# Kernel tuning notes

Measured on AMD Instinct MI355X. Metric: run time of the kernel, lower is better.

The kernel has to match this reference:

```python
import jax, jax.numpy as jnp
import numpy as np
from jax import lax

# SLAYER SRMALPHA neuron / simulation constants (from init params)
THETA = 10.0      # spike threshold
TAU_SR = 10.0     # synaptic (PSP) alpha-kernel time constant
TAU_REF = 1.0     # refractory alpha-kernel time constant
SCALE_REF = 2.0   # refractory kernel scale (x theta)
TS = 1.0          # simulation timestep


def _alpha_filter(x, tau):
    """Causal convolution of x[T, ...] with the SLAYER alpha kernel
    k[n] = (n*TS/tau) * exp(1 - n*TS/tau)  (note k[0] = 0),
    implemented as a 2-state linear recurrence (exact, O(T)).
    k[n] = c * n * a**n with a = exp(-TS/tau), c = e*TS/tau.
    """
    a = jnp.asarray(np.exp(-TS / tau), x.dtype)
    c = jnp.asarray(np.e * TS / tau, x.dtype)

    def step(carry, xn):
        p, q = carry              # p[n-1] = sum a^{n-1-m} x[m]; q[n-1] = sum (n-1-m) a^{n-1-m} x[m]
        q = a * q + a * p         # q[n]
        p = a * p + xn            # p[n]
        return (p, q), c * q      # y[n] = c*q[n]  (x[n] has weight k[0]=0)

    z = jnp.zeros_like(x[0])
    _, y = lax.scan(step, (z, z), x)
    return y


def _spike_with_refractory(u):
    """SLAYER spike: threshold membrane potential u[T, B, O]; each emitted
    spike injects the refractory alpha kernel -scaleRef*theta*(t/tauRef)*exp(1-t/tauRef)
    into the future membrane potential. Same 2-state alpha recurrence, but the
    filtered signal is the (data-dependent) spike train -> sequential scan.
    """
    a = jnp.asarray(np.exp(-TS / TAU_REF), u.dtype)
    c = jnp.asarray(-SCALE_REF * THETA * np.e * TS / TAU_REF, u.dtype)

    def step(carry, un):
        p, q = carry
        q = a * q + a * p                       # refractory trace of past spikes
        s = (un + c * q >= THETA).astype(un.dtype)
        p = a * p + s
        return (p, q), s

    z = jnp.zeros_like(u[0])
    _, s = lax.scan(step, (z, z), u)
    return s


def setup_inputs() -> dict:
    key = jax.random.key(0)
    k1, k2 = jax.random.split(key)
    B, CIN, COUT, T = 32, 1024, 1024, 500
    spike_input = (jax.random.uniform(k1, (B, CIN, 1, 1, T)) < 0.05).astype(jnp.float32)
    W = jax.random.normal(k2, (COUT, CIN), dtype=jnp.float32) * (1.0 / np.sqrt(CIN))
    return {"spike_input": spike_input, "W": W}


def reference(spike_input, W):
    B, C, _, _, T = spike_input.shape
    O = W.shape[0]
    x = spike_input.reshape(B, C, T).transpose(2, 0, 1)   # [T, B, C]
    psp = _alpha_filter(x, TAU_SR)                        # temporal PSP filter
    u = jnp.einsum('tbc,oc->tbo', psp, W)                 # slayer.dense = 1x1 conv = GEMM
    s = _spike_with_refractory(u)                         # threshold + refractory
    return s.transpose(1, 2, 0).reshape(B, O, 1, 1, T)
```

## Files before the change

kernel.cpp:

```cpp
#include <hip/hip_runtime.h>
#include <cstddef>
#include <cstdint>

#define T_DIM 500
#define B_DIM 32
#define C_DIM 1024
#define O_DIM 1024
#define M_DIM (T_DIM * B_DIM)
#define MP_DIM 16128
#define BO_DIM (B_DIM * O_DIM)

typedef __attribute__((ext_vector_type(8))) short bf16x8;
typedef __attribute__((ext_vector_type(4))) float f32x4;

static __device__ __forceinline__ ushort f2bf(float x) {
  unsigned u = __float_as_uint(x);
  return (ushort)((u + 0x7FFF + ((u >> 16) & 1)) >> 16);
}
static __device__ __forceinline__ float bf2f(ushort u) {
  return __uint_as_float(((unsigned)u) << 16);
}

static __device__ __forceinline__ bf16x8 ldsr(const ushort* p) {
  bf16x8 d;
  asm volatile("ds_read_b128 %0, %1"
               : "=v"(d)
               : "v"((unsigned)(uintptr_t)(const __attribute__((address_space(3))) ushort*)p));
  return d;
}

__global__ __launch_bounds__(256) void k_transpose(const float* __restrict__ x,
                                                   ushort* __restrict__ xt) {
  __shared__ float tile[32][33];
  const int b  = blockIdx.z;
  const int t0 = blockIdx.x * 32;
  const int c0 = blockIdx.y * 32;
  const int tx = threadIdx.x;
  const int ty = threadIdx.y;

  const int t = t0 + tx;
  if (t < T_DIM) {
#pragma unroll
    for (int r = 0; r < 4; ++r) {
      const int c = c0 + ty + r * 8;
      tile[ty + r * 8][tx] = x[((size_t)b * C_DIM + c) * T_DIM + t];
    }
  }
  __syncthreads();
#pragma unroll
  for (int r = 0; r < 4; ++r) {
    const int tt = t0 + ty + r * 8;
    if (tt < T_DIM) {
      xt[((size_t)tt * B_DIM + b) * C_DIM + c0 + tx] = f2bf(tile[tx][ty + r * 8]);
    }
  }
}

__global__ __launch_bounds__(256) void k_cast_w(const float4* __restrict__ W,
                                                ushort* __restrict__ Wb) {
  const int i = blockIdx.x * 256 + threadIdx.x;
  const float4 w = W[i];
  ushort* o = Wb + (size_t)i * 4;
  o[0] = f2bf(w.x); o[1] = f2bf(w.y); o[2] = f2bf(w.z); o[3] = f2bf(w.w);
}

__global__ __launch_bounds__(512, 2) void k_gemm_bf16(const ushort* __restrict__ A,
                                                      const ushort* __restrict__ Bw,
                                                      ushort* __restrict__ C) {
  __shared__ ushort lds[65536];

  const int tid  = threadIdx.x;
  const int wid  = tid >> 6;
  const int lane = tid & 63;

  const int orig = blockIdx.x;
  const int xcd  = orig & 7;
  const int base = (xcd < 4) ? xcd * 32 : 128 + (xcd - 4) * 31;
  const int wgid = base + (orig >> 3);
  const int row0 = (wgid >> 2) * 256;
  const int col0 = (wgid & 3) * 256;

  const int wm = wid >> 2;
  const int wn = wid & 3;

  f32x4 acc[8][4] = {};

  const int srow = wid * 16 + (lane >> 2);
  const int skof = ((lane & 3) * 8) ^ (((lane >> 5) & 1) << 4);
  const ushort* Abase = A  + (size_t)(row0 + srow) * C_DIM + skof;
  const ushort* Bbase = Bw + (size_t)(col0 + srow) * C_DIM + skof;

  const int fr  = lane & 15;
  const int fko = ((lane >> 4) * 8) ^ (((lane >> 3) & 1) << 4);
  const int aoff = wm * 8192 + fr * 32 + fko;
  const int boff = 16384 + (wn >> 1) * 8192 + (wn & 1) * 2048 + fr * 32 + fko;

#define STAGE_A(K0S, SB)                                                          \
  _Pragma("unroll")                                                               \
  for (int rh = 0; rh < 2; ++rh)                                                  \
    _Pragma("unroll")                                                             \
    for (int kh = 0; kh < 2; ++kh)                                                \
      __builtin_amdgcn_global_load_lds(                                           \
          (const __attribute__((address_space(1))) void*)(Abase + (size_t)rh * 128 * C_DIM + (K0S) + kh * 32), \
          (__attribute__((address_space(3))) void*)&lds[(SB) + rh * 8192 + kh * 4096 + wid * 512], 16, 0, 0)

#define STAGE_B(K0S, SB)                                                          \
  _Pragma("unroll")                                                               \
  for (int rh = 0; rh < 2; ++rh)                                                  \
    _Pragma("unroll")                                                             \
    for (int kh = 0; kh < 2; ++kh)                                                \
      __builtin_amdgcn_global_load_lds(                                           \
          (const __attribute__((address_space(1))) void*)(Bbase + (size_t)rh * 128 * C_DIM + (K0S) + kh * 32), \
          (__attribute__((address_space(3))) void*)&lds[(SB) + 16384 + rh * 8192 + kh * 4096 + wid * 512], 16, 0, 0)

  STAGE_A(0, 0);
  STAGE_B(0, 0);
  STAGE_A(64, 32768);
  STAGE_B(64, 32768);

  for (int t = 0; t < 16; ++t) {
    const int sb = (t & 1) * 32768;
    bf16x8 a0[4][2], a1[4][2], b0[2][2], b1[2][2];

    if (t < 15) { asm volatile("s_waitcnt vmcnt(8)" ::: "memory"); }
    else        { asm volatile("s_waitcnt vmcnt(0)" ::: "memory"); }
    __builtin_amdgcn_s_barrier();
#pragma unroll
    for (int i = 0; i < 4; ++i)
#pragma unroll
      for (int h = 0; h < 2; ++h)
        a0[i][h] = ldsr(&lds[sb + aoff + h * 4096 + i * 512]);
#pragma unroll
    for (int j = 0; j < 2; ++j)
#pragma unroll
      for (int h = 0; h < 2; ++h)
        b0[j][h] = ldsr(&lds[sb + boff + h * 4096 + j * 512]);
    asm volatile("s_waitcnt lgkmcnt(0)" ::: "memory");
    __builtin_amdgcn_sched_barrier(0);
    __builtin_amdgcn_s_setprio(1);
#pragma unroll
    for (int i = 0; i < 4; ++i)
#pragma unroll
      for (int j = 0; j < 2; ++j)
#pragma unroll
        for (int h = 0; h < 2; ++h)
          acc[i][j] = __builtin_amdgcn_mfma_f32_16x16x32_bf16(a0[i][h], b0[j][h], acc[i][j], 0, 0, 0);
    __builtin_amdgcn_s_setprio(0);
    __builtin_amdgcn_s_barrier();

#pragma unroll
    for (int i = 0; i < 4; ++i)
#pragma unroll
      for (int h = 0; h < 2; ++h)
        a1[i][h] = ldsr(&lds[sb + aoff + h * 4096 + (4 + i) * 512]);
#pragma unroll
    for (int j = 0; j < 2; ++j)
#pragma unroll
      for (int h = 0; h < 2; ++h)
        b1[j][h] = ldsr(&lds[sb + boff + h * 4096 + (2 + j) * 512]);
    asm volatile("s_waitcnt lgkmcnt(0)" ::: "memory");
    __builtin_amdgcn_sched_barrier(0);
    __builtin_amdgcn_s_setprio(1);
#pragma unroll
    for (int i = 0; i < 4; ++i)
#pragma unroll
      for (int j = 0; j < 2; ++j)
#pragma unroll
        for (int h = 0; h < 2; ++h)
          acc[4 + i][j] = __builtin_amdgcn_mfma_f32_16x16x32_bf16(a1[i][h], b0[j][h], acc[4 + i][j], 0, 0, 0);
    __builtin_amdgcn_s_setprio(0);
    __builtin_amdgcn_s_barrier();

    if (t < 14) { STAGE_A((t + 2) * 64, sb); }
    __builtin_amdgcn_s_setprio(1);
#pragma unroll
    for (int i = 0; i < 4; ++i)
#pragma unroll
      for (int j = 0; j < 2; ++j)
#pragma unroll
        for (int h = 0; h < 2; ++h)
          acc[i][2 + j] = __builtin_amdgcn_mfma_f32_16x16x32_bf16(a0[i][h], b1[j][h], acc[i][2 + j], 0, 0, 0);
    __builtin_amdgcn_s_setprio(0);
    __builtin_amdgcn_s_barrier();

    if (t < 14) { STAGE_B((t + 2) * 64, sb); }
    __builtin_amdgcn_s_setprio(1);
#pragma unroll
    for (int i = 0; i < 4; ++i)
#pragma unroll
      for (int j = 0; j < 2; ++j)
#pragma unroll
        for (int h = 0; h < 2; ++h)
          acc[4 + i][2 + j] = __builtin_amdgcn_mfma_f32_16x16x32_bf16(a1[i][h], b1[j][h], acc[4 + i][2 + j], 0, 0, 0);
    __builtin_amdgcn_s_setprio(0);
    __builtin_amdgcn_s_barrier();
  }

  const int crow = (lane >> 4) * 4;
  const int ccol = lane & 15;
#pragma unroll
  for (int i = 0; i < 8; ++i)
#pragma unroll
    for (int j = 0; j < 4; ++j) {
      ushort* cp = C + (size_t)(row0 + wm * 128 + i * 16 + crow) * O_DIM
                     + (col0 + wn * 64 + j * 16 + ccol);
#pragma unroll
      for (int r = 0; r < 4; ++r) cp[(size_t)r * O_DIM] = f2bf(acc[i][j][r]);
    }
#undef STAGE_A
#undef STAGE_B
}

__global__ __launch_bounds__(64) void k_scan(const ushort* __restrict__ v,
                                             float* __restrict__ out) {
  const int g = blockIdx.x * 64 + threadIdx.x;

  const float a1 = 0.90483741803595952f;
  const float c1 = 0.27182818284590452f;
  const float a2 = 0.36787944117144233f;
  const float c2 = -54.365636569180905f;

  float p1 = 0.f, q1 = 0.f;
  float p2 = 0.f, q2 = 0.f;

  const ushort* vp = v + g;
  float* op = out + (size_t)g * T_DIM;

  constexpr int D  = 20;
  constexpr int NC = 25;

  ushort b0[D], b1[D], b2[D];
#pragma unroll
  for (int j = 0; j < D; ++j) b0[j] = vp[(size_t)j * BO_DIM];
#pragma unroll
  for (int j = 0; j < D; ++j) b1[j] = vp[(size_t)(D + j) * BO_DIM];
#pragma unroll
  for (int j = 0; j < D; ++j) b2[j] = vp[(size_t)(2 * D + j) * BO_DIM];

#pragma unroll 5
  for (int c = 0; c < NC; ++c) {
    const int cn = (c + 3 < NC) ? (c + 3) : (NC - 1);
    ushort bn[D];
    {
      const size_t base = (size_t)cn * D;
#pragma unroll
      for (int j = 0; j < D; ++j) bn[j] = vp[(base + j) * BO_DIM];
    }

    float rr[D];
#pragma unroll
    for (int j = 0; j < D; ++j) {
      const float vn = bf2f(b0[j]);
      q1 = a1 * q1 + a1 * p1;
      p1 = a1 * p1 + vn;
      const float u = c1 * q1;
      q2 = a2 * q2 + a2 * p2;
      const float s = (u + c2 * q2 >= 10.0f) ? 1.0f : 0.0f;
      p2 = a2 * p2 + s;
      rr[j] = s;
    }

    float* o = op + c * D;
#pragma unroll
    for (int j = 0; j < D; j += 4)
      *(float4*)&o[j] = make_float4(rr[j], rr[j + 1], rr[j + 2], rr[j + 3]);

#pragma unroll
    for (int j = 0; j < D; ++j) { b0[j] = b1[j]; b1[j] = b2[j]; b2[j] = bn[j]; }
  }
}

extern "C" void kernel_launch(void* const* d_in, const int* in_sizes, int n_in,
                              void* d_out, int out_size, void* d_ws, size_t ws_size,
                              hipStream_t stream) {
  const float* x = (const float*)d_in[0];
  const float* W = (const float*)d_in[1];
  float* out = (float*)d_out;

  ushort* v  = (ushort*)d_ws;
  ushort* xt = v + (size_t)MP_DIM * O_DIM;
  ushort* Wb = xt + (size_t)MP_DIM * C_DIM;

  dim3 g0((T_DIM + 31) / 32, C_DIM / 32, B_DIM);
  k_transpose<<<g0, dim3(32, 8), 0, stream>>>(x, xt);

  k_cast_w<<<(O_DIM * C_DIM / 4) / 256, 256, 0, stream>>>((const float4*)W, Wb);

  k_gemm_bf16<<<(MP_DIM / 256) * (O_DIM / 256), 512, 0, stream>>>(xt, Wb, v);

  k_scan<<<BO_DIM / 64, 64, 0, stream>>>(v, out);
}
```

Baseline: 90.05 us.

## Double GEMM workgroup to 1024 threads and coalesce scan output via LDS bitmasks

The GEMM keeps its 256x256 tile but splits it across 16 waves instead of 8. Each wave now owns 64x64 outputs, which halves the accumulator registers and issues one K-half load per thread. The scan packs spike bits into per-thread LDS words and then writes each output row cooperatively, so the scattered per-thread stores of stride-500 rows become coalesced float4 writes. Costs include more barrier participants, the launch-bounds request of 1024 threads with 4 blocks (which LDS size cannot actually satisfy), and a clamped tail read in the scan.

```diff
diff --git a/kernel.cpp b/kernel.cpp
--- a/kernel.cpp
+++ b/kernel.cpp
@@ -64,9 +64,9 @@
   o[0] = f2bf(w.x); o[1] = f2bf(w.y); o[2] = f2bf(w.z); o[3] = f2bf(w.w);
 }
 
-__global__ __launch_bounds__(512, 2) void k_gemm_bf16(const ushort* __restrict__ A,
-                                                      const ushort* __restrict__ Bw,
-                                                      ushort* __restrict__ C) {
+__global__ __launch_bounds__(1024, 4) void k_gemm_bf16(const ushort* __restrict__ A,
+                                                       const ushort* __restrict__ Bw,
+                                                       ushort* __restrict__ C) {
   __shared__ ushort lds[65536];
 
   const int tid  = threadIdx.x;
@@ -83,35 +83,32 @@
   const int wm = wid >> 2;
   const int wn = wid & 3;
 
-  f32x4 acc[8][4] = {};
-
-  const int srow = wid * 16 + (lane >> 2);
-  const int skof = ((lane & 3) * 8) ^ (((lane >> 5) & 1) << 4);
-  const ushort* Abase = A  + (size_t)(row0 + srow) * C_DIM + skof;
-  const ushort* Bbase = Bw + (size_t)(col0 + srow) * C_DIM + skof;
+  f32x4 acc[4][4] = {};
+
+  const int kh  = tid >> 9;
+  const int rin = (tid >> 2) & 127;
+  const int sk  = ((tid & 3) * 8) ^ (((tid >> 5) & 1) << 4);
+  const ushort* Abase = A  + (size_t)(row0 + rin) * C_DIM + kh * 32 + sk;
+  const ushort* Bbase = Bw + (size_t)(col0 + rin) * C_DIM + kh * 32 + sk;
 
   const int fr  = lane & 15;
   const int fko = ((lane >> 4) * 8) ^ (((lane >> 3) & 1) << 4);
-  const int aoff = wm * 8192 + fr * 32 + fko;
-  const int boff = 16384 + (wn >> 1) * 8192 + (wn & 1) * 2048 + fr * 32 + fko;
+  const int aoff = (wm >> 1) * 8192 + ((wm & 1) * 64 + fr) * 32 + fko;
+  const int boff = 16384 + (wn >> 1) * 8192 + ((wn & 1) * 64 + fr) * 32 + fko;
 
 #define STAGE_A(K0S, SB)                                                          \
   _Pragma("unroll")                                                               \
   for (int rh = 0; rh < 2; ++rh)                                                  \
-    _Pragma("unroll")                                                             \
-    for (int kh = 0; kh < 2; ++kh)                                                \
-      __builtin_amdgcn_global_load_lds(                                           \
-          (const __attribute__((address_space(1))) void*)(Abase + (size_t)rh * 128 * C_DIM + (K0S) + kh * 32), \
-          (__attribute__((address_space(3))) void*)&lds[(SB) + rh * 8192 + kh * 4096 + wid * 512], 16, 0, 0)
+    __builtin_amdgcn_global_load_lds(                                             \
+        (const __attribute__((address_space(1))) void*)(Abase + (size_t)rh * 128 * C_DIM + (K0S)), \
+        (__attribute__((address_space(3))) void*)&lds[(SB) + rh * 8192 + wid * 512], 16, 0, 0)
 
 #define STAGE_B(K0S, SB)                                                          \
   _Pragma("unroll")                                                               \
   for (int rh = 0; rh < 2; ++rh)                                                  \
-    _Pragma("unroll")                                                             \
-    for (int kh = 0; kh < 2; ++kh)                                                \
-      __builtin_amdgcn_global_load_lds(                                           \
-          (const __attribute__((address_space(1))) void*)(Bbase + (size_t)rh * 128 * C_DIM + (K0S) + kh * 32), \
-          (__attribute__((address_space(3))) void*)&lds[(SB) + 16384 + rh * 8192 + kh * 4096 + wid * 512], 16, 0, 0)
+    __builtin_amdgcn_global_load_lds(                                             \
+        (const __attribute__((address_space(1))) void*)(Bbase + (size_t)rh * 128 * C_DIM + (K0S)), \
+        (__attribute__((address_space(3))) void*)&lds[(SB) + 16384 + rh * 8192 + wid * 512], 16, 0, 0)
 
   STAGE_A(0, 0);
   STAGE_B(0, 0);
@@ -120,16 +117,16 @@
 
   for (int t = 0; t < 16; ++t) {
     const int sb = (t & 1) * 32768;
-    bf16x8 a0[4][2], a1[4][2], b0[2][2], b1[2][2];
-
-    if (t < 15) { asm volatile("s_waitcnt vmcnt(8)" ::: "memory"); }
+    bf16x8 a[4][2], b0[2][2], b1[2][2];
+
+    if (t < 15) { asm volatile("s_waitcnt vmcnt(4)" ::: "memory"); }
     else        { asm volatile("s_waitcnt vmcnt(0)" ::: "memory"); }
     __builtin_amdgcn_s_barrier();
 #pragma unroll
     for (int i = 0; i < 4; ++i)
 #pragma unroll
       for (int h = 0; h < 2; ++h)
-        a0[i][h] = ldsr(&lds[sb + aoff + h * 4096 + i * 512]);
+        a[i][h] = ldsr(&lds[sb + aoff + h * 4096 + i * 512]);
 #pragma unroll
     for (int j = 0; j < 2; ++j)
 #pragma unroll
@@ -139,20 +136,15 @@
     __builtin_amdgcn_sched_barrier(0);
     __builtin_amdgcn_s_setprio(1);
 #pragma unroll
-    for (int i = 0; i < 4; ++i)
+    for (int i = 0; i < 2; ++i)
 #pragma unroll
       for (int j = 0; j < 2; ++j)
 #pragma unroll
         for (int h = 0; h < 2; ++h)
-          acc[i][j] = __builtin_amdgcn_mfma_f32_16x16x32_bf16(a0[i][h], b0[j][h], acc[i][j], 0, 0, 0);
+          acc[i][j] = __builtin_amdgcn_mfma_f32_16x16x32_bf16(a[i][h], b0[j][h], acc[i][j], 0, 0, 0);
     __builtin_amdgcn_s_setprio(0);
     __builtin_amdgcn_s_barrier();
 
-#pragma unroll
-    for (int i = 0; i < 4; ++i)
-#pragma unroll
-      for (int h = 0; h < 2; ++h)
-        a1[i][h] = ldsr(&lds[sb + aoff + h * 4096 + (4 + i) * 512]);
 #pragma unroll
     for (int j = 0; j < 2; ++j)
 #pragma unroll
@@ -162,36 +154,36 @@
     __builtin_amdgcn_sched_barrier(0);
     __builtin_amdgcn_s_setprio(1);
 #pragma unroll
-    for (int i = 0; i < 4; ++i)
+    for (int i = 2; i < 4; ++i)
 #pragma unroll
       for (int j = 0; j < 2; ++j)
 #pragma unroll
         for (int h = 0; h < 2; ++h)
-          acc[4 + i][j] = __builtin_amdgcn_mfma_f32_16x16x32_bf16(a1[i][h], b0[j][h], acc[4 + i][j], 0, 0, 0);
+          acc[i][j] = __builtin_amdgcn_mfma_f32_16x16x32_bf16(a[i][h], b0[j][h], acc[i][j], 0, 0, 0);
     __builtin_amdgcn_s_setprio(0);
     __builtin_amdgcn_s_barrier();
 
     if (t < 14) { STAGE_A((t + 2) * 64, sb); }
     __builtin_amdgcn_s_setprio(1);
 #pragma unroll
-    for (int i = 0; i < 4; ++i)
+    for (int i = 0; i < 2; ++i)
 #pragma unroll
       for (int j = 0; j < 2; ++j)
 #pragma unroll
         for (int h = 0; h < 2; ++h)
-          acc[i][2 + j] = __builtin_amdgcn_mfma_f32_16x16x32_bf16(a0[i][h], b1[j][h], acc[i][2 + j], 0, 0, 0);
+          acc[i][2 + j] = __builtin_amdgcn_mfma_f32_16x16x32_bf16(a[i][h], b1[j][h], acc[i][2 + j], 0, 0, 0);
     __builtin_amdgcn_s_setprio(0);
     __builtin_amdgcn_s_barrier();
 
     if (t < 14) { STAGE_B((t + 2) * 64, sb); }
     __builtin_amdgcn_s_setprio(1);
 #pragma unroll
-    for (int i = 0; i < 4; ++i)
+    for (int i = 2; i < 4; ++i)
 #pragma unroll
       for (int j = 0; j < 2; ++j)
 #pragma unroll
         for (int h = 0; h < 2; ++h)
-          acc[4 + i][2 + j] = __builtin_amdgcn_mfma_f32_16x16x32_bf16(a1[i][h], b1[j][h], acc[4 + i][2 + j], 0, 0, 0);
+          acc[i][2 + j] = __builtin_amdgcn_mfma_f32_16x16x32_bf16(a[i][h], b1[j][h], acc[i][2 + j], 0, 0, 0);
     __builtin_amdgcn_s_setprio(0);
     __builtin_amdgcn_s_barrier();
   }
@@ -199,10 +191,10 @@
   const int crow = (lane >> 4) * 4;
   const int ccol = lane & 15;
 #pragma unroll
-  for (int i = 0; i < 8; ++i)
+  for (int i = 0; i < 4; ++i)
 #pragma unroll
     for (int j = 0; j < 4; ++j) {
-      ushort* cp = C + (size_t)(row0 + wm * 128 + i * 16 + crow) * O_DIM
+      ushort* cp = C + (size_t)(row0 + wm * 64 + i * 16 + crow) * O_DIM
                      + (col0 + wn * 64 + j * 16 + ccol);
 #pragma unroll
       for (int r = 0; r < 4; ++r) cp[(size_t)r * O_DIM] = f2bf(acc[i][j][r]);
@@ -213,7 +205,9 @@
 
 __global__ __launch_bounds__(64) void k_scan(const ushort* __restrict__ v,
                                              float* __restrict__ out) {
-  const int g = blockIdx.x * 64 + threadIdx.x;
+  __shared__ unsigned wbits[64][16];
+  const int l  = threadIdx.x;
+  const int g0 = blockIdx.x * 64;
 
   const float a1 = 0.90483741803595952f;
   const float c1 = 0.27182818284590452f;
@@ -223,11 +217,10 @@
   float p1 = 0.f, q1 = 0.f;
   float p2 = 0.f, q2 = 0.f;
 
-  const ushort* vp = v + g;
-  float* op = out + (size_t)g * T_DIM;
-
-  constexpr int D  = 20;
-  constexpr int NC = 25;
+  const ushort* vp = v + g0 + l;
+
+  constexpr int D  = 32;
+  constexpr int NC = 16;
 
   ushort b0[D], b1[D], b2[D];
 #pragma unroll
@@ -237,17 +230,18 @@
 #pragma unroll
   for (int j = 0; j < D; ++j) b2[j] = vp[(size_t)(2 * D + j) * BO_DIM];
 
-#pragma unroll 5
+#pragma unroll 4
   for (int c = 0; c < NC; ++c) {
     const int cn = (c + 3 < NC) ? (c + 3) : (NC - 1);
     ushort bn[D];
-    {
-      const size_t base = (size_t)cn * D;
-#pragma unroll
-      for (int j = 0; j < D; ++j) bn[j] = vp[(base + j) * BO_DIM];
-    }
-
-    float rr[D];
+#pragma unroll
+    for (int j = 0; j < D; ++j) {
+      int t = cn * D + j;
+      if (t > 499) t = 499;
+      bn[j] = vp[(size_t)t * BO_DIM];
+    }
+
+    unsigned curw = 0;
 #pragma unroll
     for (int j = 0; j < D; ++j) {
       const float vn = bf2f(b0[j]);
@@ -255,18 +249,34 @@
       p1 = a1 * p1 + vn;
       const float u = c1 * q1;
       q2 = a2 * q2 + a2 * p2;
-      const float s = (u + c2 * q2 >= 10.0f) ? 1.0f : 0.0f;
-      p2 = a2 * p2 + s;
-      rr[j] = s;
-    }
-
-    float* o = op + c * D;
-#pragma unroll
-    for (int j = 0; j < D; j += 4)
-      *(float4*)&o[j] = make_float4(rr[j], rr[j + 1], rr[j + 2], rr[j + 3]);
+      const bool fire = (u + c2 * q2 >= 10.0f);
+      p2 = a2 * p2 + (fire ? 1.0f : 0.0f);
+      curw |= (unsigned)fire << j;
+    }
+    wbits[l][c] = curw;
 
 #pragma unroll
     for (int j = 0; j < D; ++j) { b0[j] = b1[j]; b1[j] = b2[j]; b2[j] = bn[j]; }
+  }
+  __syncthreads();
+
+  for (int r = 0; r < 64; ++r) {
+    float* orow = out + (size_t)(g0 + r) * T_DIM;
+#pragma unroll
+    for (int wv = 0; wv < 2; ++wv) {
+      const int w = wv * 64 + l;
+      if (w < 125) {
+        const int t0 = w * 4;
+        const unsigned word = wbits[r][t0 >> 5];
+        const unsigned sh = (unsigned)(t0 & 31);
+        float4 f;
+        f.x = ((word >> (sh + 0)) & 1u) ? 1.0f : 0.0f;
+        f.y = ((word >> (sh + 1)) & 1u) ? 1.0f : 0.0f;
+        f.z = ((word >> (sh + 2)) & 1u) ? 1.0f : 0.0f;
+        f.w = ((word >> (sh + 3)) & 1u) ? 1.0f : 0.0f;
+        *(float4*)&orow[t0] = f;
+      }
+    }
   }
 }
 
@@ -286,7 +296,7 @@
 
   k_cast_w<<<(O_DIM * C_DIM / 4) / 256, 256, 0, stream>>>((const float4*)W, Wb);
 
-  k_gemm_bf16<<<(MP_DIM / 256) * (O_DIM / 256), 512, 0, stream>>>(xt, Wb, v);
+  k_gemm_bf16<<<(MP_DIM / 256) * (O_DIM / 256), 1024, 0, stream>>>(xt, Wb, v);
 
   k_scan<<<BO_DIM / 64, 64, 0, stream>>>(v, out);
 }
```

Result: slower. 137.6 us (+52.8%).
